# Kernel tuning notes

Measured on AMD Instinct MI355X. Metric: run time of the kernel, lower is better.

## Reference

```python
import jax, jax.numpy as jnp
import numpy as np

N_ITER = 2
N_NEIGHBOR = 8
NEG = -9.0e15


def _rel_transform(emb, rel, W_rel):
    # emb: [..., d] neighbor embeddings, rel: [...] relation ids.
    # Original applies tanh(W_r @ e) to entries whose relation == r (all entries
    # are covered since rel in [0, n_relation)). Small fixed loop over relations.
    out = jnp.zeros_like(emb)
    for r in range(W_rel.shape[0]):
        y = jnp.tanh(jnp.einsum('...d,ed->...e', emb, W_rel[r]))  # Linear(bias=False): x @ W.T
        out = out + jnp.where((rel == r)[..., None], y, jnp.zeros_like(y))
    return out


def _masked_softmax(s):
    s = jnp.where(s == 0, NEG, s)
    return jax.nn.softmax(s, axis=-1)


def _forward(user_indices, item_indices, entity_emb, W_rel, adj_entity,
             adj_relation, items_clicked, num_clicked, labels_table, offset):
    bs = user_indices.shape[0]
    dim = entity_emb.shape[1]
    n_old = adj_entity.shape[1]

    # user embedding = sum of clicked item embeddings * 1/num_clicked
    hist = items_clicked[user_indices]                              # [bs, H]
    user_emb = entity_emb[hist].sum(axis=1) * (1.0 / num_clicked[user_indices])[:, None]
    user_emb4 = user_emb.reshape(bs, 1, 1, dim)

    seeds = item_indices.reshape(bs, 1, 1)
    entities = [seeds]
    entities_emb = [entity_emb[seeds]]                              # [bs,1,1,d]
    scores_us = []
    for i in range(N_ITER):
        nbr_e = adj_entity[entities[i]].reshape(bs, -1, n_old)      # [bs,N,64]
        nbr_r = adj_relation[entities[i]].reshape(bs, -1, n_old)
        nbr_emb = _rel_transform(entity_emb[nbr_e], nbr_r, W_rel)   # [bs,N,64,d]
        s = jnp.mean(user_emb4 * nbr_emb, axis=-1)                  # [bs,N,64]
        s = _masked_softmax(s)
        s_top, ids = jax.lax.top_k(s, N_NEIGHBOR)                   # sort desc + slice
        s_top = _masked_softmax(s_top)
        scores_us.append(s_top)                                     # [bs,N,K]
        nbr_e = jnp.take_along_axis(nbr_e, ids, axis=-1)
        nbr_r = jnp.take_along_axis(nbr_r, ids, axis=-1)
        nbr_emb = _rel_transform(entity_emb[nbr_e], nbr_r, W_rel)   # [bs,N,K,d]
        entities.append(nbr_e)
        entities_emb.append(nbr_emb)

    # label propagation setup (dense stand-in for the TF hash table; 0.5 = missing)
    entity_labels, reset_masks = [], []
    holdout = None
    for ent in entities:
        ent2 = ent.reshape(bs, -1)
        concat = user_indices[:, None] * offset + ent2
        if holdout is None:
            holdout = concat
        lab = labels_table[user_indices[:, None], ent2]
        holdout_mask = (holdout - concat) != 0
        reset_mask = (lab != 0.5) & holdout_mask
        lab = jnp.where(holdout_mask, lab, jnp.asarray(0.5, lab.dtype))
        entity_labels.append(lab)
        reset_masks.append(reset_mask)
    reset_masks = reset_masks[:-1]

    for i in range(N_ITER):
        next_emb, next_lab = [], []
        for hop in range(N_ITER - i):
            agg = jnp.mean(scores_us[hop][..., None] * entities_emb[hop + 1],
                           axis=2, keepdims=True).reshape(entities_emb[hop].shape)
            lab_agg = jnp.sum(scores_us[hop] *
                              entity_labels[hop + 1].reshape(bs, -1, N_NEIGHBOR), axis=-1)
            lab_out = jnp.where(reset_masks[hop], entity_labels[hop], lab_agg)
            act = jnp.tanh if i == N_ITER - 1 else jax.nn.relu
            next_emb.append(act(agg + entities_emb[hop]))
            next_lab.append(lab_out)
        entities_emb, entity_labels = next_emb, next_lab

    pred_labels = entity_labels[0].reshape(bs)
    item_out = entities_emb[0].reshape(bs, dim)
    scores = jax.nn.sigmoid(jnp.sum(user_emb * item_out, axis=1))
    pred_labels = jax.nn.sigmoid(pred_labels - 0.5)
    return scores, pred_labels


def setup_inputs() -> dict:
    key = jax.random.key(0)
    ks = jax.random.split(key, 10)
    n_user, n_entity, n_rel, dim = 1024, 50000, 8, 64
    n_old, hist, bs = 64, 50, 1024
    entity_emb = jax.random.normal(ks[0], (n_entity + 1, dim), jnp.float32) * 0.1
    entity_emb = entity_emb.at[-1].set(0.0)  # padding_idx row
    W_rel = jax.random.normal(ks[1], (n_rel, dim, dim), jnp.float32) / np.float32(np.sqrt(dim))
    adj_entity = jax.random.randint(ks[2], (n_entity + 1, n_old), 0, n_entity)
    adj_relation = jax.random.randint(ks[3], (n_entity + 1, n_old), 0, n_rel)
    items_clicked = jax.random.randint(ks[4], (n_user, hist), 0, n_entity + 1)
    num_clicked = jax.random.uniform(ks[5], (n_user,), jnp.float32, 1.0, float(hist))
    labels_table = jax.random.choice(ks[6], jnp.array([0.0, 0.5, 1.0], jnp.float32),
                                     (n_user, n_entity + 1))
    user_indices = jax.random.randint(ks[7], (bs,), 0, n_user)
    item_indices = jax.random.randint(ks[8], (bs,), 0, n_entity)
    return dict(user_indices=user_indices, item_indices=item_indices,
                entity_emb=entity_emb, W_rel=W_rel, adj_entity=adj_entity,
                adj_relation=adj_relation, items_clicked=items_clicked,
                num_clicked=num_clicked, labels_table=labels_table,
                offset=n_entity + 1)


def reference(user_indices, item_indices, entity_emb, W_rel, adj_entity,
              adj_relation, items_clicked, num_clicked, labels_table, offset):
    return _forward(user_indices, item_indices, entity_emb, W_rel, adj_entity,
                    adj_relation, items_clicked, num_clicked, labels_table, offset)
```

## Files before the change

### kernel.cpp

```cpp
#include <hip/hip_runtime.h>
#include <math.h>

#define NEGV -9000000000000000.0f
#define WPB 16
#define NTHR 1024

struct LdsW {
  float4 w[8 * 16 * 64];
  float xb[WPB][64];
};

__device__ __forceinline__ float wave_sum(float v) {
#pragma unroll
  for (int m = 32; m; m >>= 1) v += __shfl_xor(v, m, 64);
  return v;
}

__device__ __forceinline__ int rl(int v, int l) {
  return __builtin_amdgcn_readlane(v, l);
}

__device__ __forceinline__ void stage_W(float4* wl, const float* __restrict__ W) {
  const float4* Wg = (const float4*)W;
  for (int f = threadIdx.x; f < 8192; f += NTHR) {
    float4 v = Wg[f];
    int r = f >> 10, e = (f >> 4) & 63, k = f & 15;
    wl[(((r << 4) + k) << 6) + e] = v;
  }
  __syncthreads();
}

__device__ __forceinline__ void load_xu_hi(const float* __restrict__ emb, int nb,
                                           float4 xu[8]) {
  const float4* xg = (const float4*)(emb + ((size_t)nb << 6) + 32);
#pragma unroll
  for (int j = 0; j < 8; ++j) xu[j] = xg[j];
}

__device__ __forceinline__ void load_xu_full(const float* __restrict__ emb, int nb,
                                             float4 xu[16]) {
  const float4* xg = (const float4*)(emb + ((size_t)nb << 6));
#pragma unroll
  for (int j = 0; j < 16; ++j) xu[j] = xg[j];
}

__device__ __forceinline__ float transform_pre(const float4 xu[16], int r, int lane,
                                               const float4* wl) {
  const float4* wr = wl + (r << 10) + lane;
  float acc = 0.f;
#pragma unroll
  for (int k = 0; k < 16; ++k) {
    float4 w = wr[k << 6];
    acc = fmaf(w.x, xu[k].x, acc);
    acc = fmaf(w.y, xu[k].y, acc);
    acc = fmaf(w.z, xu[k].z, acc);
    acc = fmaf(w.w, xu[k].w, acc);
  }
  return tanhf(acc);
}

__device__ __forceinline__ void score_step(int pos, int lane, const float4* wl,
                                           float* xbuf, const float* __restrict__ emb,
                                           int srt_r, int srt_nb, int order, float u_e,
                                           float4 wv[16], int& rcur, float& xv,
                                           float& s_mine, float4 xu[8]) {
  int r = rl(srt_r, pos);
  if (r != rcur) {
    const float4* wr = wl + (r << 10) + lane;
#pragma unroll
    for (int k = 0; k < 16; ++k) wv[k] = wr[k << 6];
#pragma unroll
    for (int k = 0; k < 16; ++k)
      asm volatile("" : "+v"(wv[k].x), "+v"(wv[k].y), "+v"(wv[k].z), "+v"(wv[k].w));
    rcur = r;
  }
  int nbn = (pos < 63) ? rl(srt_nb, pos + 1) : 0;
  __builtin_amdgcn_wave_barrier();
  xbuf[lane] = xv;
  __builtin_amdgcn_wave_barrier();
  float xnext = 0.f;
  if (pos < 63) xnext = emb[((size_t)nbn << 6) + lane];
  asm volatile("s_waitcnt lgkmcnt(0)" ::: "memory");
  __builtin_amdgcn_wave_barrier();
  float acc = 0.f;
#pragma unroll
  for (int k = 0; k < 8; ++k) {
    float4 x = *(const float4*)(xbuf + 4 * k);
    acc = fmaf(wv[k].x, x.x, acc);
    acc = fmaf(wv[k].y, x.y, acc);
    acc = fmaf(wv[k].z, x.z, acc);
    acc = fmaf(wv[k].w, x.w, acc);
  }
#pragma unroll
  for (int k = 8; k < 16; ++k) {
    acc = fmaf(wv[k].x, xu[k - 8].x, acc);
    acc = fmaf(wv[k].y, xu[k - 8].y, acc);
    acc = fmaf(wv[k].z, xu[k - 8].z, acc);
    acc = fmaf(wv[k].w, xu[k - 8].w, acc);
  }
  if (pos < 63) load_xu_hi(emb, nbn, xu);
  float y = tanhf(acc);
  float totv = wave_sum(u_e * y);
  int n = rl(order, pos);
  if (lane == n) s_mine = totv * (1.0f / 64.0f);
  xv = xnext;
}

__device__ __forceinline__ void score_select(int eid, int b, int lane,
                                             const float* __restrict__ emb,
                                             const float4* wl, float* xbuf,
                                             const int* __restrict__ adjE,
                                             const int* __restrict__ adjR,
                                             const float* __restrict__ user_emb,
                                             int& nbr, int& rel, int seli[8],
                                             float wout[8]) {
  nbr = adjE[((size_t)eid << 6) + lane];
  rel = adjR[((size_t)eid << 6) + lane];
  float u_e = user_emb[((size_t)b << 6) + lane];
  int myrank = 0, basec = 0;
  unsigned long long ltmask = (1ull << lane) - 1ull;
#pragma unroll
  for (int rr = 0; rr < 8; ++rr) {
    unsigned long long m = __ballot(rel == rr);
    if (rel == rr) myrank = basec + (int)__popcll(m & ltmask);
    basec += (int)__popcll(m);
  }
  int order = __builtin_amdgcn_ds_permute(myrank << 2, lane);
  int srt_nb = __shfl(nbr, order, 64);
  int srt_r = __shfl(rel, order, 64);

  int nb0 = rl(srt_nb, 0);
  float xv = emb[((size_t)nb0 << 6) + lane];
  float4 xu[8];
  load_xu_hi(emb, nb0, xu);
  float4 wv[16];
  int rcur = -1;
  float s_mine = 0.f;
  for (int pos = 0; pos < 64; ++pos)
    score_step(pos, lane, wl, xbuf, emb, srt_r, srt_nb, order, u_e, wv, rcur, xv,
               s_mine, xu);
  float sv = (s_mine == 0.0f) ? NEGV : s_mine;
  float mx = sv;
#pragma unroll
  for (int m = 32; m; m >>= 1) mx = fmaxf(mx, __shfl_xor(mx, m, 64));
  float p = expf(sv - mx);
  float Z = wave_sum(p);
  p /= Z;
  float v = p;
  int vi = lane;
  float selv[8];
#pragma unroll
  for (int j = 0; j < 8; ++j) {
    float bv = v;
    int bi = vi;
#pragma unroll
    for (int m = 1; m < 64; m <<= 1) {
      float ov = __shfl_xor(bv, m, 64);
      int oi = __shfl_xor(bi, m, 64);
      if (ov > bv || (ov == bv && oi < bi)) { bv = ov; bi = oi; }
    }
    selv[j] = bv;
    seli[j] = bi;
    if (lane == bi) v = -__builtin_inff();
  }
  float m8 = -__builtin_inff();
#pragma unroll
  for (int j = 0; j < 8; ++j) {
    float tt = (selv[j] == 0.f) ? NEGV : selv[j];
    selv[j] = tt;
    m8 = fmaxf(m8, tt);
  }
  float Z8 = 0.f;
#pragma unroll
  for (int j = 0; j < 8; ++j) {
    selv[j] = expf(selv[j] - m8);
    Z8 += selv[j];
  }
#pragma unroll
  for (int j = 0; j < 8; ++j) wout[j] = selv[j] / Z8;
}

__global__ __launch_bounds__(256) void k_user(const int* __restrict__ ui,
                                              const float* __restrict__ emb,
                                              const int* __restrict__ clicked,
                                              const float* __restrict__ numc, int hist,
                                              float* __restrict__ user_emb, int ntask) {
  int w = threadIdx.x >> 6, lane = threadIdx.x & 63;
  int b = blockIdx.x * 4 + w;
  if (b >= ntask) return;
  int u = ui[b];
  float acc = 0.f;
  for (int h = 0; h < hist; ++h) {
    int it = clicked[u * hist + h];
    acc += emb[((size_t)it << 6) + lane];
  }
  user_emb[((size_t)b << 6) + lane] = acc * (1.0f / numc[u]);
}

__global__ __launch_bounds__(NTHR, 4) void k_hop0_f(
    const int* __restrict__ ii, const float* __restrict__ emb,
    const float* __restrict__ W, const int* __restrict__ adjE,
    const int* __restrict__ adjR, const float* __restrict__ user_emb,
    int* __restrict__ e1, float* __restrict__ s0w, float* __restrict__ emb1,
    int ntask) {
  __shared__ LdsW S;
  stage_W(S.w, W);
  int w = threadIdx.x >> 6, lane = threadIdx.x & 63;
  int tot = gridDim.x * WPB;
  for (int t = blockIdx.x + gridDim.x * w; t < ntask; t += tot) {
    int eid = ii[t];
    int nbr, rel, seli[8];
    float w8[8];
    score_select(eid, t, lane, emb, S.w, S.xb[w], adjE, adjR, user_emb, nbr, rel, seli,
                 w8);
    int nbs[8], rrs[8];
#pragma unroll
    for (int j = 0; j < 8; ++j) {
      int sj = __builtin_amdgcn_readfirstlane(seli[j]);
      nbs[j] = rl(nbr, sj);
      rrs[j] = rl(rel, sj);
    }
    float4 xtA[16], xtB[16];
    load_xu_full(emb, nbs[0], xtA);
#pragma unroll
    for (int j = 0; j < 8; ++j) {
      const float4* xc = (j & 1) ? xtB : xtA;
      float4* xn = (j & 1) ? xtA : xtB;
      if (j < 7) load_xu_full(emb, nbs[j + 1], xn);
      float y = transform_pre(xc, rrs[j], lane, S.w);
      emb1[(((size_t)t * 8 + j) << 6) + lane] = y;
      if (lane == 0) {
        e1[t * 8 + j] = nbs[j];
        s0w[t * 8 + j] = w8[j];
      }
    }
  }
}

__global__ __launch_bounds__(NTHR, 4) void k_hop1_f(
    const int* __restrict__ ui, const int* __restrict__ ii, const float* __restrict__ emb,
    const float* __restrict__ W, const int* __restrict__ adjE,
    const int* __restrict__ adjR, const float* __restrict__ labels, int np1,
    const float* __restrict__ user_emb, const int* __restrict__ e1,
    const float* __restrict__ emb1, float* __restrict__ emb1p,
    float* __restrict__ lab1p, int ntask) {
  __shared__ LdsW S;
  stage_W(S.w, W);
  int w = threadIdx.x >> 6, lane = threadIdx.x & 63;
  int wid = blockIdx.x * WPB + w;
  int tot = gridDim.x * WPB;
  for (int bj = wid; bj < ntask; bj += tot) {
    int b = bj >> 3;
    int u = ui[b];
    int item = ii[b];
    int eid = e1[bj];
    int nbr, rel, seli[8];
    float w8[8];
    score_select(eid, b, lane, emb, S.w, S.xb[w], adjE, adjR, user_emb, nbr, rel, seli,
                 w8);
    int nbs[8], rrs[8];
#pragma unroll
    for (int k = 0; k < 8; ++k) {
      int sk = __builtin_amdgcn_readfirstlane(seli[k]);
      nbs[k] = rl(nbr, sk);
      rrs[k] = rl(rel, sk);
    }
    float4 xtA[16], xtB[16];
    load_xu_full(emb, nbs[0], xtA);
    float agg = 0.f, labagg = 0.f;
#pragma unroll
    for (int k = 0; k < 8; ++k) {
      const float4* xc = (k & 1) ? xtB : xtA;
      float4* xn = (k & 1) ? xtA : xtB;
      if (k < 7) load_xu_full(emb, nbs[k + 1], xn);
      float y = transform_pre(xc, rrs[k], lane, S.w);
      agg = fmaf(w8[k], y, agg);
      float raw2 = labels[(size_t)u * np1 + nbs[k]];
      float lab2 = (nbs[k] != item) ? raw2 : 0.5f;
      labagg = fmaf(w8[k], lab2, labagg);
    }
    float base = emb1[((size_t)bj << 6) + lane];
    emb1p[((size_t)bj << 6) + lane] = fmaxf(fmaf(agg, 0.125f, base), 0.f);
    if (lane == 0) {
      float raw1 = labels[(size_t)u * np1 + eid];
      bool hm = (eid != item);
      float l1 = hm ? raw1 : 0.5f;
      bool reset1 = (raw1 != 0.5f) && hm;
      lab1p[bj] = reset1 ? l1 : labagg;
    }
  }
}

__global__ __launch_bounds__(256) void k_final(const int* __restrict__ ii,
                                               const float* __restrict__ emb,
                                               const float* __restrict__ user_emb,
                                               const float* __restrict__ s0,
                                               const float* __restrict__ emb1,
                                               const float* __restrict__ emb1p,
                                               const float* __restrict__ lab1p,
                                               float* __restrict__ out, int bs) {
  int w = threadIdx.x >> 6, lane = threadIdx.x & 63;
  int b = blockIdx.x * 4 + w;
  if (b >= bs) return;
  int item = ii[b];
  float ue = user_emb[((size_t)b << 6) + lane];
  float agg = 0.f, aggp = 0.f, lab = 0.f;
#pragma unroll
  for (int j = 0; j < 8; ++j) {
    float s = s0[b * 8 + j];
    agg = fmaf(s, emb1[(((size_t)b * 8 + j) << 6) + lane], agg);
    aggp = fmaf(s, emb1p[(((size_t)b * 8 + j) << 6) + lane], aggp);
    lab = fmaf(s, lab1p[b * 8 + j], lab);
  }
  float e0 = emb[((size_t)item << 6) + lane];
  float h = fmaxf(fmaf(agg, 0.125f, e0), 0.f);
  float h2 = tanhf(fmaf(aggp, 0.125f, h));
  float dot = wave_sum(ue * h2);
  if (lane == 0) {
    out[b] = 1.f / (1.f + expf(-dot));
    out[bs + b] = 1.f / (1.f + expf(-(lab - 0.5f)));
  }
}

extern "C" void kernel_launch(void* const* d_in, const int* in_sizes, int n_in, void* d_out,
                              int out_size, void* d_ws, size_t ws_size, hipStream_t stream) {
  const int* ui = (const int*)d_in[0];
  const int* ii = (const int*)d_in[1];
  const float* emb = (const float*)d_in[2];
  const float* W = (const float*)d_in[3];
  const int* adjE = (const int*)d_in[4];
  const int* adjR = (const int*)d_in[5];
  const int* clicked = (const int*)d_in[6];
  const float* numc = (const float*)d_in[7];
  const float* labels = (const float*)d_in[8];

  int bs = in_sizes[0];
  int np1 = in_sizes[2] / 64;
  int nuser = in_sizes[7];
  int hist = in_sizes[6] / nuser;

  float* user_emb = (float*)d_ws;
  float* s0w = user_emb + (size_t)bs * 64;
  int* e1 = (int*)(s0w + (size_t)bs * 8);
  float* emb1 = (float*)(e1 + (size_t)bs * 8);
  float* emb1p = emb1 + (size_t)bs * 8 * 64;
  float* lab1p = emb1p + (size_t)bs * 8 * 64;

  int nt0 = bs;
  int nt1 = bs * 8;

  k_user<<<(nt0 + 3) / 4, 256, 0, stream>>>(ui, emb, clicked, numc, hist, user_emb, nt0);
  k_hop0_f<<<256, NTHR, 0, stream>>>(ii, emb, W, adjE, adjR, user_emb, e1, s0w, emb1,
                                     nt0);
  k_hop1_f<<<256, NTHR, 0, stream>>>(ui, ii, emb, W, adjE, adjR, labels, np1, user_emb,
                                     e1, emb1, emb1p, lab1p, nt1);
  k_final<<<(nt0 + 3) / 4, 256, 0, stream>>>(ii, emb, user_emb, s0w, emb1, emb1p, lab1p,
                                             (float*)d_out, bs);
}
```

Before: 213.7 us.

## Split hop-0 neighbor scoring across four waves per seed item

Hop 0 now assigns four waves to each seed item instead of one wave per item. Each wave scores a 16-neighbor slice, and the partial scores are combined through shared memory. Each wave then runs the top-k selection redundantly and transforms two of the eight selected neighbors. This spreads the serial 64-step scoring chain of the small hop-0 task count over more waves to cut latency. In exchange it adds a block barrier, repeats top-k work in every wave, and launches bs/4 blocks that each stage the full W matrix into LDS.

```diff
diff --git a/kernel.cpp b/kernel.cpp
--- a/kernel.cpp
+++ b/kernel.cpp
@@ -59,9 +59,10 @@
   return tanhf(acc);
 }
 
-__device__ __forceinline__ void score_step(int pos, int lane, const float4* wl,
-                                           float* xbuf, const float* __restrict__ emb,
-                                           int srt_r, int srt_nb, int order, float u_e,
+__device__ __forceinline__ void score_step(int pos, int pend, int lane,
+                                           const float4* wl, float* xbuf,
+                                           const float* __restrict__ emb, int srt_r,
+                                           int srt_nb, int order, float u_e,
                                            float4 wv[16], int& rcur, float& xv,
                                            float& s_mine, float4 xu[8]) {
   int r = rl(srt_r, pos);
@@ -74,12 +75,12 @@
       asm volatile("" : "+v"(wv[k].x), "+v"(wv[k].y), "+v"(wv[k].z), "+v"(wv[k].w));
     rcur = r;
   }
-  int nbn = (pos < 63) ? rl(srt_nb, pos + 1) : 0;
+  int nbn = (pos < pend - 1) ? rl(srt_nb, pos + 1) : 0;
   __builtin_amdgcn_wave_barrier();
   xbuf[lane] = xv;
   __builtin_amdgcn_wave_barrier();
   float xnext = 0.f;
-  if (pos < 63) xnext = emb[((size_t)nbn << 6) + lane];
+  if (pos < pend - 1) xnext = emb[((size_t)nbn << 6) + lane];
   asm volatile("s_waitcnt lgkmcnt(0)" ::: "memory");
   __builtin_amdgcn_wave_barrier();
   float acc = 0.f;
@@ -98,7 +99,7 @@
     acc = fmaf(wv[k].z, xu[k - 8].z, acc);
     acc = fmaf(wv[k].w, xu[k - 8].w, acc);
   }
-  if (pos < 63) load_xu_hi(emb, nbn, xu);
+  if (pos < pend - 1) load_xu_hi(emb, nbn, xu);
   float y = tanhf(acc);
   float totv = wave_sum(u_e * y);
   int n = rl(order, pos);
@@ -106,14 +107,13 @@
   xv = xnext;
 }
 
-__device__ __forceinline__ void score_select(int eid, int b, int lane,
-                                             const float* __restrict__ emb,
-                                             const float4* wl, float* xbuf,
-                                             const int* __restrict__ adjE,
-                                             const int* __restrict__ adjR,
-                                             const float* __restrict__ user_emb,
-                                             int& nbr, int& rel, int seli[8],
-                                             float wout[8]) {
+__device__ __forceinline__ void score_partial(int eid, int b, int lane, int p0, int cnt,
+                                              const float* __restrict__ emb,
+                                              const float4* wl, float* xbuf,
+                                              const int* __restrict__ adjE,
+                                              const int* __restrict__ adjR,
+                                              const float* __restrict__ user_emb,
+                                              int& nbr, int& rel, float& s_mine) {
   nbr = adjE[((size_t)eid << 6) + lane];
   rel = adjR[((size_t)eid << 6) + lane];
   float u_e = user_emb[((size_t)b << 6) + lane];
@@ -129,16 +129,21 @@
   int srt_nb = __shfl(nbr, order, 64);
   int srt_r = __shfl(rel, order, 64);
 
-  int nb0 = rl(srt_nb, 0);
+  int pend = p0 + cnt;
+  int nb0 = rl(srt_nb, p0);
   float xv = emb[((size_t)nb0 << 6) + lane];
   float4 xu[8];
   load_xu_hi(emb, nb0, xu);
   float4 wv[16];
   int rcur = -1;
-  float s_mine = 0.f;
-  for (int pos = 0; pos < 64; ++pos)
-    score_step(pos, lane, wl, xbuf, emb, srt_r, srt_nb, order, u_e, wv, rcur, xv,
+  s_mine = 0.f;
+  for (int pos = p0; pos < pend; ++pos)
+    score_step(pos, pend, lane, wl, xbuf, emb, srt_r, srt_nb, order, u_e, wv, rcur, xv,
                s_mine, xu);
+}
+
+__device__ __forceinline__ void topsel_core(float s_mine, int lane, int seli[8],
+                                            float wout[8]) {
   float sv = (s_mine == 0.0f) ? NEGV : s_mine;
   float mx = sv;
 #pragma unroll
@@ -204,35 +209,47 @@
     int* __restrict__ e1, float* __restrict__ s0w, float* __restrict__ emb1,
     int ntask) {
   __shared__ LdsW S;
+  __shared__ __align__(16) float sb[4][4][64];
   stage_W(S.w, W);
   int w = threadIdx.x >> 6, lane = threadIdx.x & 63;
-  int tot = gridDim.x * WPB;
-  for (int t = blockIdx.x + gridDim.x * w; t < ntask; t += tot) {
-    int eid = ii[t];
-    int nbr, rel, seli[8];
-    float w8[8];
-    score_select(eid, t, lane, emb, S.w, S.xb[w], adjE, adjR, user_emb, nbr, rel, seli,
-                 w8);
-    int nbs[8], rrs[8];
+  int tq = w & 3;
+  int tib = w >> 2;
+  int t = blockIdx.x * 4 + tib;
+  bool active = t < ntask;
+  int tc = active ? t : (ntask - 1);
+  int eid = ii[tc];
+  int nbr, rel;
+  float s_part;
+  score_partial(eid, tc, lane, tq * 16, 16, emb, S.w, S.xb[w], adjE, adjR, user_emb,
+                nbr, rel, s_part);
+  sb[tib][tq][lane] = s_part;
+  __syncthreads();
+  float s_mine =
+      ((sb[tib][0][lane] + sb[tib][1][lane]) + sb[tib][2][lane]) + sb[tib][3][lane];
+  int seli[8];
+  float w8[8];
+  topsel_core(s_mine, lane, seli, w8);
+  if (!active) return;
+  int nbs[8], rrs[8];
+#pragma unroll
+  for (int j = 0; j < 8; ++j) {
+    int sj = __builtin_amdgcn_readfirstlane(seli[j]);
+    nbs[j] = rl(nbr, sj);
+    rrs[j] = rl(rel, sj);
+  }
+  int j0 = tq * 2;
+  float4 xtA[16], xtB[16];
+  load_xu_full(emb, nbs[j0], xtA);
+  load_xu_full(emb, nbs[j0 + 1], xtB);
+  float y0 = transform_pre(xtA, rrs[j0], lane, S.w);
+  emb1[(((size_t)t * 8 + j0) << 6) + lane] = y0;
+  float y1 = transform_pre(xtB, rrs[j0 + 1], lane, S.w);
+  emb1[(((size_t)t * 8 + j0 + 1) << 6) + lane] = y1;
+  if (lane == 0 && tq == 0) {
 #pragma unroll
     for (int j = 0; j < 8; ++j) {
-      int sj = __builtin_amdgcn_readfirstlane(seli[j]);
-      nbs[j] = rl(nbr, sj);
-      rrs[j] = rl(rel, sj);
-    }
-    float4 xtA[16], xtB[16];
-    load_xu_full(emb, nbs[0], xtA);
-#pragma unroll
-    for (int j = 0; j < 8; ++j) {
-      const float4* xc = (j & 1) ? xtB : xtA;
-      float4* xn = (j & 1) ? xtA : xtB;
-      if (j < 7) load_xu_full(emb, nbs[j + 1], xn);
-      float y = transform_pre(xc, rrs[j], lane, S.w);
-      emb1[(((size_t)t * 8 + j) << 6) + lane] = y;
-      if (lane == 0) {
-        e1[t * 8 + j] = nbs[j];
-        s0w[t * 8 + j] = w8[j];
-      }
+      e1[t * 8 + j] = nbs[j];
+      s0w[t * 8 + j] = w8[j];
     }
   }
 }
@@ -254,10 +271,13 @@
     int u = ui[b];
     int item = ii[b];
     int eid = e1[bj];
-    int nbr, rel, seli[8];
+    int nbr, rel;
+    float s_mine;
+    score_partial(eid, b, lane, 0, 64, emb, S.w, S.xb[w], adjE, adjR, user_emb, nbr,
+                  rel, s_mine);
+    int seli[8];
     float w8[8];
-    score_select(eid, b, lane, emb, S.w, S.xb[w], adjE, adjR, user_emb, nbr, rel, seli,
-                 w8);
+    topsel_core(s_mine, lane, seli, w8);
     int nbs[8], rrs[8];
 #pragma unroll
     for (int k = 0; k < 8; ++k) {
@@ -350,8 +370,8 @@
   int nt1 = bs * 8;
 
   k_user<<<(nt0 + 3) / 4, 256, 0, stream>>>(ui, emb, clicked, numc, hist, user_emb, nt0);
-  k_hop0_f<<<256, NTHR, 0, stream>>>(ii, emb, W, adjE, adjR, user_emb, e1, s0w, emb1,
-                                     nt0);
+  k_hop0_f<<<(nt0 + 3) / 4, NTHR, 0, stream>>>(ii, emb, W, adjE, adjR, user_emb, e1, s0w,
+                                               emb1, nt0);
   k_hop1_f<<<256, NTHR, 0, stream>>>(ui, ii, emb, W, adjE, adjR, labels, np1, user_emb,
                                      e1, emb1, emb1p, lab1p, nt1);
   k_final<<<(nt0 + 3) / 4, 256, 0, stream>>>(ii, emb, user_emb, s0w, emb1, emb1p, lab1p,
```

Result: slower. 424.2 us (+98.5%).

## Split hop-0 scoring across four waves per seed with separate select kernel

Applied to the files above, without the earlier changes.

Hop-0 scoring of the 64 neighbours per seed item is split over four waves, each handling 16 sorted positions and writing partial per-lane scores to a workspace buffer. A new select kernel sums the partials and does the top-k, softmax and transform of the selected neighbours. The goal is more parallelism in hop 0, where only bs tasks previously ran one wave each, leaving the GPU underfilled. The cost is an extra kernel launch, the partial-score round trip through global memory, and each extra wave redoing the relation sort and restaging W into LDS.

```diff
diff --git a/kernel.cpp b/kernel.cpp
--- a/kernel.cpp
+++ b/kernel.cpp
@@ -59,9 +59,25 @@
   return tanhf(acc);
 }
 
-__device__ __forceinline__ void score_step(int pos, int lane, const float4* wl,
-                                           float* xbuf, const float* __restrict__ emb,
-                                           int srt_r, int srt_nb, int order, float u_e,
+__device__ __forceinline__ void sort_order(int lane, int nbr, int rel, int& order,
+                                           int& srt_nb, int& srt_r) {
+  int myrank = 0, basec = 0;
+  unsigned long long ltmask = (1ull << lane) - 1ull;
+#pragma unroll
+  for (int rr = 0; rr < 8; ++rr) {
+    unsigned long long m = __ballot(rel == rr);
+    if (rel == rr) myrank = basec + (int)__popcll(m & ltmask);
+    basec += (int)__popcll(m);
+  }
+  order = __builtin_amdgcn_ds_permute(myrank << 2, lane);
+  srt_nb = __shfl(nbr, order, 64);
+  srt_r = __shfl(rel, order, 64);
+}
+
+__device__ __forceinline__ void score_step(int pos, int pend, int lane,
+                                           const float4* wl, float* xbuf,
+                                           const float* __restrict__ emb, int srt_r,
+                                           int srt_nb, int order, float u_e,
                                            float4 wv[16], int& rcur, float& xv,
                                            float& s_mine, float4 xu[8]) {
   int r = rl(srt_r, pos);
@@ -74,12 +90,12 @@
       asm volatile("" : "+v"(wv[k].x), "+v"(wv[k].y), "+v"(wv[k].z), "+v"(wv[k].w));
     rcur = r;
   }
-  int nbn = (pos < 63) ? rl(srt_nb, pos + 1) : 0;
+  int nbn = (pos < pend - 1) ? rl(srt_nb, pos + 1) : 0;
   __builtin_amdgcn_wave_barrier();
   xbuf[lane] = xv;
   __builtin_amdgcn_wave_barrier();
   float xnext = 0.f;
-  if (pos < 63) xnext = emb[((size_t)nbn << 6) + lane];
+  if (pos < pend - 1) xnext = emb[((size_t)nbn << 6) + lane];
   asm volatile("s_waitcnt lgkmcnt(0)" ::: "memory");
   __builtin_amdgcn_wave_barrier();
   float acc = 0.f;
@@ -98,7 +114,7 @@
     acc = fmaf(wv[k].z, xu[k - 8].z, acc);
     acc = fmaf(wv[k].w, xu[k - 8].w, acc);
   }
-  if (pos < 63) load_xu_hi(emb, nbn, xu);
+  if (pos < pend - 1) load_xu_hi(emb, nbn, xu);
   float y = tanhf(acc);
   float totv = wave_sum(u_e * y);
   int n = rl(order, pos);
@@ -106,39 +122,8 @@
   xv = xnext;
 }
 
-__device__ __forceinline__ void score_select(int eid, int b, int lane,
-                                             const float* __restrict__ emb,
-                                             const float4* wl, float* xbuf,
-                                             const int* __restrict__ adjE,
-                                             const int* __restrict__ adjR,
-                                             const float* __restrict__ user_emb,
-                                             int& nbr, int& rel, int seli[8],
-                                             float wout[8]) {
-  nbr = adjE[((size_t)eid << 6) + lane];
-  rel = adjR[((size_t)eid << 6) + lane];
-  float u_e = user_emb[((size_t)b << 6) + lane];
-  int myrank = 0, basec = 0;
-  unsigned long long ltmask = (1ull << lane) - 1ull;
-#pragma unroll
-  for (int rr = 0; rr < 8; ++rr) {
-    unsigned long long m = __ballot(rel == rr);
-    if (rel == rr) myrank = basec + (int)__popcll(m & ltmask);
-    basec += (int)__popcll(m);
-  }
-  int order = __builtin_amdgcn_ds_permute(myrank << 2, lane);
-  int srt_nb = __shfl(nbr, order, 64);
-  int srt_r = __shfl(rel, order, 64);
-
-  int nb0 = rl(srt_nb, 0);
-  float xv = emb[((size_t)nb0 << 6) + lane];
-  float4 xu[8];
-  load_xu_hi(emb, nb0, xu);
-  float4 wv[16];
-  int rcur = -1;
-  float s_mine = 0.f;
-  for (int pos = 0; pos < 64; ++pos)
-    score_step(pos, lane, wl, xbuf, emb, srt_r, srt_nb, order, u_e, wv, rcur, xv,
-               s_mine, xu);
+__device__ __forceinline__ void topsel_core(float s_mine, int lane, int seli[8],
+                                            float wout[8]) {
   float sv = (s_mine == 0.0f) ? NEGV : s_mine;
   float mx = sv;
 #pragma unroll
@@ -197,10 +182,41 @@
   user_emb[((size_t)b << 6) + lane] = acc * (1.0f / numc[u]);
 }
 
-__global__ __launch_bounds__(NTHR, 4) void k_hop0_f(
+__global__ __launch_bounds__(NTHR, 4) void k_score0(
     const int* __restrict__ ii, const float* __restrict__ emb,
     const float* __restrict__ W, const int* __restrict__ adjE,
     const int* __restrict__ adjR, const float* __restrict__ user_emb,
+    float* __restrict__ spart, int ntask) {
+  __shared__ LdsW S;
+  stage_W(S.w, W);
+  int w = threadIdx.x >> 6, lane = threadIdx.x & 63;
+  int gw = blockIdx.x * WPB + w;
+  if (gw >= ntask * 4) return;
+  int t = gw >> 2, q = gw & 3;
+  int eid = ii[t];
+  int nbr = adjE[((size_t)eid << 6) + lane];
+  int rel = adjR[((size_t)eid << 6) + lane];
+  float u_e = user_emb[((size_t)t << 6) + lane];
+  int order, srt_nb, srt_r;
+  sort_order(lane, nbr, rel, order, srt_nb, srt_r);
+  int p0 = q * 16, pend = p0 + 16;
+  int nb0 = rl(srt_nb, p0);
+  float xv = emb[((size_t)nb0 << 6) + lane];
+  float4 xu[8];
+  load_xu_hi(emb, nb0, xu);
+  float4 wv[16];
+  int rcur = -1;
+  float s_mine = 0.f;
+  for (int pos = p0; pos < pend; ++pos)
+    score_step(pos, pend, lane, S.w, S.xb[w], emb, srt_r, srt_nb, order, u_e, wv, rcur,
+               xv, s_mine, xu);
+  spart[((size_t)gw << 6) + lane] = s_mine;
+}
+
+__global__ __launch_bounds__(NTHR, 4) void k_sel0(
+    const int* __restrict__ ii, const float* __restrict__ emb,
+    const float* __restrict__ W, const int* __restrict__ adjE,
+    const int* __restrict__ adjR, const float* __restrict__ spart,
     int* __restrict__ e1, float* __restrict__ s0w, float* __restrict__ emb1,
     int ntask) {
   __shared__ LdsW S;
@@ -209,16 +225,26 @@
   int tot = gridDim.x * WPB;
   for (int t = blockIdx.x + gridDim.x * w; t < ntask; t += tot) {
     int eid = ii[t];
-    int nbr, rel, seli[8];
+    int nbr = adjE[((size_t)eid << 6) + lane];
+    int rel = adjR[((size_t)eid << 6) + lane];
+    const float* sp = spart + ((size_t)t << 8);
+    float s_mine = ((sp[lane] + sp[64 + lane]) + sp[128 + lane]) + sp[192 + lane];
+    int seli[8];
     float w8[8];
-    score_select(eid, t, lane, emb, S.w, S.xb[w], adjE, adjR, user_emb, nbr, rel, seli,
-                 w8);
+    topsel_core(s_mine, lane, seli, w8);
     int nbs[8], rrs[8];
 #pragma unroll
     for (int j = 0; j < 8; ++j) {
       int sj = __builtin_amdgcn_readfirstlane(seli[j]);
       nbs[j] = rl(nbr, sj);
       rrs[j] = rl(rel, sj);
+    }
+    if (lane == 0) {
+#pragma unroll
+      for (int j = 0; j < 8; ++j) {
+        e1[t * 8 + j] = nbs[j];
+        s0w[t * 8 + j] = w8[j];
+      }
     }
     float4 xtA[16], xtB[16];
     load_xu_full(emb, nbs[0], xtA);
@@ -229,10 +255,6 @@
       if (j < 7) load_xu_full(emb, nbs[j + 1], xn);
       float y = transform_pre(xc, rrs[j], lane, S.w);
       emb1[(((size_t)t * 8 + j) << 6) + lane] = y;
-      if (lane == 0) {
-        e1[t * 8 + j] = nbs[j];
-        s0w[t * 8 + j] = w8[j];
-      }
     }
   }
 }
@@ -254,10 +276,24 @@
     int u = ui[b];
     int item = ii[b];
     int eid = e1[bj];
-    int nbr, rel, seli[8];
+    int nbr = adjE[((size_t)eid << 6) + lane];
+    int rel = adjR[((size_t)eid << 6) + lane];
+    float u_e = user_emb[((size_t)b << 6) + lane];
+    int order, srt_nb, srt_r;
+    sort_order(lane, nbr, rel, order, srt_nb, srt_r);
+    int nb0 = rl(srt_nb, 0);
+    float xv = emb[((size_t)nb0 << 6) + lane];
+    float4 xu[8];
+    load_xu_hi(emb, nb0, xu);
+    float4 wv[16];
+    int rcur = -1;
+    float s_mine = 0.f;
+    for (int pos = 0; pos < 64; ++pos)
+      score_step(pos, 64, lane, S.w, S.xb[w], emb, srt_r, srt_nb, order, u_e, wv, rcur,
+                 xv, s_mine, xu);
+    int seli[8];
     float w8[8];
-    score_select(eid, b, lane, emb, S.w, S.xb[w], adjE, adjR, user_emb, nbr, rel, seli,
-                 w8);
+    topsel_core(s_mine, lane, seli, w8);
     int nbs[8], rrs[8];
 #pragma unroll
     for (int k = 0; k < 8; ++k) {
@@ -345,13 +381,15 @@
   float* emb1 = (float*)(e1 + (size_t)bs * 8);
   float* emb1p = emb1 + (size_t)bs * 8 * 64;
   float* lab1p = emb1p + (size_t)bs * 8 * 64;
+  float* spart = lab1p + (size_t)bs * 8;
 
   int nt0 = bs;
   int nt1 = bs * 8;
 
   k_user<<<(nt0 + 3) / 4, 256, 0, stream>>>(ui, emb, clicked, numc, hist, user_emb, nt0);
-  k_hop0_f<<<256, NTHR, 0, stream>>>(ii, emb, W, adjE, adjR, user_emb, e1, s0w, emb1,
-                                     nt0);
+  k_score0<<<(nt0 * 4 + WPB - 1) / WPB, NTHR, 0, stream>>>(ii, emb, W, adjE, adjR,
+                                                           user_emb, spart, nt0);
+  k_sel0<<<256, NTHR, 0, stream>>>(ii, emb, W, adjE, adjR, spart, e1, s0w, emb1, nt0);
   k_hop1_f<<<256, NTHR, 0, stream>>>(ui, ii, emb, W, adjE, adjR, labels, np1, user_emb,
                                      e1, emb1, emb1p, lab1p, nt1);
   k_final<<<(nt0 + 3) / 4, 256, 0, stream>>>(ii, emb, user_emb, s0w, emb1, emb1p, lab1p,
```

Result: slower. 423.9 us (+98.3%).
